# Optimization experiments

Hardware: AMD Instinct MI355X
Metric: run time of the kernel (lower is better)

## Reference

```python
import jax, jax.numpy as jnp
import numpy as np

T, B, D, U = 256, 128, 1024, 1024

def _orthogonal(key, shape, gain=1.0, dtype=jnp.float32):
    # Orthogonal init matching tf.initializers.Orthogonal
    n_rows, n_cols = shape
    big = max(n_rows, n_cols)
    a = jax.random.normal(key, (big, min(n_rows, n_cols)), dtype=jnp.float32)
    q, r = jnp.linalg.qr(a)
    q = q * jnp.sign(jnp.diag(r))
    q = q[:n_rows, :n_cols] if n_rows >= n_cols else q.T[:n_rows, :n_cols]
    return (gain * q).astype(dtype)

def setup_inputs() -> dict:
    key = jax.random.key(0)
    k1, k2, k3, k4 = jax.random.split(key, 4)
    inputs = jax.random.normal(k1, (T, B, D), dtype=jnp.float32)
    states = jnp.zeros((2, B, U), dtype=jnp.float32)  # stacked (c, h)
    masks = jax.random.randint(k2, (T, B), 0, 2).astype(jnp.int32)
    kernelx = _orthogonal(k3, (D, 4 * U), gain=1.0)
    kernelh = _orthogonal(k4, (U, 4 * U), gain=1.0)
    bias = jnp.zeros((4 * U,), dtype=jnp.float32)
    return {"inputs": inputs, "states": states, "masks": masks,
            "kernelx": kernelx, "kernelh": kernelh, "bias": bias}

def reference(inputs, states, masks, kernelx, kernelh, bias):
    c0, h0 = states[0], states[1]
    # mask semantics from source: m = 1 - masks; state is zeroed where mask==1
    m = (1.0 - masks.astype(inputs.dtype))[..., None]       # [T, B, 1]
    # Precompute input contribution for all steps (one big GEMM)
    xz = jnp.einsum('tbd,dk->tbk', inputs, kernelx) + bias  # [T, B, 4U]

    def step(carry, xs):
        c, h = carry
        xz_t, m_t = xs
        c = c * m_t
        h = h * m_t
        z = xz_t + h @ kernelh                              # [B, 4U]
        i, f, o, u = jnp.split(z, 4, axis=-1)
        i = jax.nn.sigmoid(i)
        f = jax.nn.sigmoid(f)
        o = jax.nn.sigmoid(o)
        u = jnp.tanh(u)
        c = f * c + i * u
        h = o * jnp.tanh(c)
        return (c, h), h

    (c, h), out = jax.lax.scan(step, (c0, h0), (xz, m))
    return out, jnp.stack([c, h])
```

## Files before the change

### kernel.cpp

```cpp
#include <hip/hip_runtime.h>


typedef float  f32x4 __attribute__((ext_vector_type(4)));
typedef float  f32x2 __attribute__((ext_vector_type(2)));
typedef __bf16 bf16x8 __attribute__((ext_vector_type(8)));
typedef unsigned short us8 __attribute__((ext_vector_type(8)));
typedef unsigned short us4 __attribute__((ext_vector_type(4)));
typedef unsigned int   u32x4 __attribute__((ext_vector_type(4)));

#define TT 256
#define BB 128
#define DD 1024
#define UU 1024
#define NZ 4096

typedef __attribute__((address_space(3))) unsigned       lds_u32;
typedef const __attribute__((address_space(1))) unsigned glob_u32;

__device__ __forceinline__ unsigned short f2bf(float x) {
  union { float f; unsigned u; } v; v.f = x;
  unsigned r = v.u + 0x7fffu + ((v.u >> 16) & 1u);
  return (unsigned short)(r >> 16);
}
__device__ __forceinline__ float bf2f(unsigned short b) {
  union { unsigned u; float f; } v; v.u = ((unsigned)b) << 16;
  return v.f;
}
__device__ __forceinline__ float sigm(float x) { return 1.f / (1.f + __expf(-x)); }
__device__ __forceinline__ float tanh_(float x) { return 1.f - 2.f / (__expf(2.f * x) + 1.f); }

__global__ __launch_bounds__(256) void k_convert(const float* __restrict__ in,
                                                 unsigned short* __restrict__ out,
                                                 int n8) {
  int i = blockIdx.x * 256 + threadIdx.x;
  if (i >= n8) return;
  const float4 a = *(const float4*)(in + (size_t)i * 8);
  const float4 b = *(const float4*)(in + (size_t)i * 8 + 4);
  us8 v;
  v[0] = f2bf(a.x); v[1] = f2bf(a.y); v[2] = f2bf(a.z); v[3] = f2bf(a.w);
  v[4] = f2bf(b.x); v[5] = f2bf(b.y); v[6] = f2bf(b.z); v[7] = f2bf(b.w);
  *(us8*)(out + (size_t)i * 8) = v;
}

__global__ __launch_bounds__(256) void k_transpose(const float* __restrict__ in,
                                                   unsigned short* __restrict__ out) {
  __shared__ unsigned short tile[64][72];
  const int ni = blockIdx.x;
  const int ki = blockIdx.y;
  const int t = threadIdx.x;
  const int c = t & 63, r0 = t >> 6;
#pragma unroll
  for (int rr = 0; rr < 16; ++rr) {
    int r = r0 * 16 + rr;
    tile[r][c] = f2bf(in[(size_t)(ki * 64 + r) * NZ + ni * 64 + c]);
  }
  __syncthreads();
  const int kcol = t & 63, ng = t >> 6;
#pragma unroll
  for (int cc = 0; cc < 16; ++cc) {
    int n_off = ng * 16 + cc;
    out[(size_t)(ni * 64 + n_off) * DD + ki * 64 + kcol] = tile[kcol][n_off];
  }
}

__global__ __launch_bounds__(256, 2) void k_gemm_bf(const unsigned short* __restrict__ A,
                                                    const unsigned short* __restrict__ Bt,
                                                    unsigned short* __restrict__ C) {
  __shared__ unsigned short Al[2][128 * 64];
  __shared__ unsigned short Bl[2][128 * 64];
  const int bx = blockIdx.x;
  const int wgid = (bx & 7) * 1024 + (bx >> 3);
  const int tm = wgid >> 5, tn = wgid & 31;
  const int tid = threadIdx.x;
  const int wave = tid >> 6, lane = tid & 63;
  const int wr = wave >> 1, wc = wave & 1;
  const int l15 = lane & 15, kg = lane >> 4;

  f32x4 acc[4][4] = {};

  const int srow = tid >> 3;
  const int scol = (tid & 7) * 8;
  const unsigned sdst = tid * 8;

  auto stage = [&](int buf, int kt) {
#pragma unroll
    for (int i = 0; i < 4; ++i) {
      __builtin_amdgcn_global_load_lds(
          (glob_u32*)(A  + (size_t)(tm * 128 + i * 32 + srow) * DD + kt * 64 + scol),
          (lds_u32*)&Al[buf][i * 2048 + sdst], 16, 0, 0);
      __builtin_amdgcn_global_load_lds(
          (glob_u32*)(Bt + (size_t)(tn * 128 + i * 32 + srow) * DD + kt * 64 + scol),
          (lds_u32*)&Bl[buf][i * 2048 + sdst], 16, 0, 0);
    }
  };

  stage(0, 0);
  __syncthreads();

  for (int kt = 0; kt < 16; ++kt) {
    const int buf = kt & 1;
    if (kt < 15) stage(buf ^ 1, kt + 1);
#pragma unroll
    for (int ks = 0; ks < 2; ++ks) {
      bf16x8 af[4], bfr[4];
#pragma unroll
      for (int mi = 0; mi < 4; ++mi)
        af[mi] = *(const bf16x8*)&Al[buf][(wr * 64 + mi * 16 + l15) * 64 + ks * 32 + kg * 8];
#pragma unroll
      for (int ni = 0; ni < 4; ++ni)
        bfr[ni] = *(const bf16x8*)&Bl[buf][(wc * 64 + ni * 16 + l15) * 64 + ks * 32 + kg * 8];
#pragma unroll
      for (int mi = 0; mi < 4; ++mi)
#pragma unroll
        for (int ni = 0; ni < 4; ++ni)
          acc[ni][mi] = __builtin_amdgcn_mfma_f32_16x16x32_bf16(bfr[ni], af[mi], acc[ni][mi], 0, 0, 0);
    }
    __syncthreads();
  }

#pragma unroll
  for (int mi = 0; mi < 4; ++mi) {
    const size_t row = (size_t)tm * 128 + wr * 64 + mi * 16 + l15;
#pragma unroll
    for (int ni = 0; ni < 4; ++ni) {
      const size_t col = (size_t)tn * 128 + wc * 64 + ni * 16 + kg * 4;
      us4 v;
      v[0] = f2bf(acc[ni][mi][0]); v[1] = f2bf(acc[ni][mi][1]);
      v[2] = f2bf(acc[ni][mi][2]); v[3] = f2bf(acc[ni][mi][3]);
      *(us4*)(C + row * NZ + col) = v;
    }
  }
}

__global__ __launch_bounds__(256, 1) void k_scan(const float* __restrict__ init_cs,
                                                 const int* __restrict__ masks,
                                                 const unsigned short* __restrict__ WhT,
                                                 const float* __restrict__ bias,
                                                 const unsigned short* __restrict__ xz,
                                                 float* __restrict__ out,
                                                 unsigned short* __restrict__ hglob,
                                                 unsigned* __restrict__ flags) {
  __shared__ char  hlds_c[32768];
  __shared__ float zlds[4][16][33];
  __shared__ int   mlds[TT * 16 + 16];

  const int tid = threadIdx.x;
  const int wave = tid >> 6, lane = tid & 63;
  const int l15 = lane & 15, kg = lane >> 4;
  const int blk = blockIdx.x;
  const int g = blk & 7;
  const int sb = blk >> 3;
  const int u0 = sb * 32;
  const int row0 = g * 16;
  unsigned* fl = flags + g * 64;

  u32x4 w0[32], w1[32];
  {
    const size_t r0 = (size_t)(wave * UU + u0 + l15) * DD;
    const size_t r1 = (size_t)(wave * UU + u0 + 16 + l15) * DD;
#pragma unroll
    for (int ks = 0; ks < 32; ++ks) {
      w0[ks] = *(const u32x4*)(WhT + r0 + ks * 32 + kg * 8);
      w1[ks] = *(const u32x4*)(WhT + r1 + ks * 32 + kg * 8);
    }
#pragma unroll
    for (int ks = 0; ks < 32; ++ks) {
      asm volatile("" : "+v"(w0[ks]));
      asm volatile("" : "+v"(w1[ks]));
    }
  }

  for (int i = 0; i < 16; ++i) {
    int idx = i * 256 + tid;
    mlds[idx] = masks[(size_t)(idx >> 4) * BB + row0 + (idx & 15)];
  }
  if (tid < 16) mlds[TT * 16 + tid] = 0;

  const int er = tid >> 4;
  const int ec = (tid & 15) * 2;
  const int grow = row0 + er;
  const int guu = u0 + ec;

  float bs0[4], bs1[4];
#pragma unroll
  for (int gt = 0; gt < 4; ++gt) {
    bs0[gt] = bias[gt * UU + guu];
    bs1[gt] = bias[gt * UU + guu + 1];
  }

  float cv0 = init_cs[(size_t)grow * UU + guu];
  float cv1 = init_cs[(size_t)grow * UU + guu + 1];
  float hv0 = init_cs[(size_t)BB * UU + grow * UU + guu];
  float hv1 = init_cs[(size_t)BB * UU + grow * UU + guu + 1];

  const unsigned wswz = ((unsigned)(er & 7)) << 4;
  const unsigned hoff = (unsigned)er * 2048u + ((((unsigned)guu) * 2u) ^ wswz);

  {
    int m0 = masks[grow];
    float s = m0 ? 0.f : 1.f;
    char* base = (char*)hglob + (size_t)g * 32768 + hoff;
    unsigned pv = ((unsigned)f2bf(hv1 * s) << 16) | f2bf(hv0 * s);
    *(unsigned*)base = pv;
  }
  __syncthreads();
  if (tid == 0) fl[sb] = 1;
  if (wave == 0) {
    unsigned v;
    do { v = __hip_atomic_load(&fl[lane & 31], __ATOMIC_RELAXED, __HIP_MEMORY_SCOPE_AGENT); }
    while (!__all(v >= 1));
  }
  __syncthreads();

  const unsigned rswz = ((unsigned)(l15 & 7)) << 4;
  const char* hp0 = hlds_c + l15 * 2048 + (((unsigned)(kg * 16 + 0)) ^ rswz);
  const char* hp1 = hlds_c + l15 * 2048 + (((unsigned)(kg * 16 + 64)) ^ rswz);

  for (int t = 0; t < TT; ++t) {
    {
      const char* gsrc = (const char*)hglob + ((size_t)((t & 1) * 8 + g)) * 32768;
      u32x4 sv[8];
#pragma unroll
      for (int i = 0; i < 8; ++i) {
        const char* ap = gsrc + (i * 256 + tid) * 16;
        asm volatile("global_load_dwordx4 %0, %1, off sc0" : "=v"(sv[i]) : "v"(ap));
      }
      asm volatile("s_waitcnt vmcnt(0)" ::: "memory");
      __builtin_amdgcn_sched_barrier(0);
#pragma unroll
      for (int i = 0; i < 8; ++i)
        *(u32x4*)(hlds_c + (i * 256 + tid) * 16) = sv[i];
    }
    __syncthreads();

    unsigned xzv[4];
    {
      const size_t xrow = ((size_t)(t * BB + grow)) * NZ;
#pragma unroll
      for (int gt = 0; gt < 4; ++gt)
        xzv[gt] = *(const unsigned*)(xz + xrow + gt * UU + guu);
    }

    f32x4 acc0 = {0.f, 0.f, 0.f, 0.f};
    f32x4 acc1 = {0.f, 0.f, 0.f, 0.f};
#pragma unroll
    for (int ks = 0; ks < 32; ++ks) {
      const char* p = ((ks & 1) ? hp1 : hp0) + (ks >> 1) * 128;
      bf16x8 a = *(const bf16x8*)p;
      acc0 = __builtin_amdgcn_mfma_f32_16x16x32_bf16(a, __builtin_bit_cast(bf16x8, w0[ks]), acc0, 0, 0, 0);
      acc1 = __builtin_amdgcn_mfma_f32_16x16x32_bf16(a, __builtin_bit_cast(bf16x8, w1[ks]), acc1, 0, 0, 0);
    }

#pragma unroll
    for (int j = 0; j < 4; ++j) {
      zlds[wave][kg * 4 + j][l15] = acc0[j];
      zlds[wave][kg * 4 + j][16 + l15] = acc1[j];
    }
    __syncthreads();

    const int mcur = mlds[t * 16 + er];
    const int mnxt = mlds[(t + 1) * 16 + er];
    float z0[4], z1[4];
#pragma unroll
    for (int gt = 0; gt < 4; ++gt) {
      z0[gt] = zlds[gt][er][ec]     + bs0[gt] + bf2f((unsigned short)(xzv[gt] & 0xffffu));
      z1[gt] = zlds[gt][er][ec + 1] + bs1[gt] + bf2f((unsigned short)(xzv[gt] >> 16));
    }
    const float sm = mcur ? 0.f : 1.f;
    cv0 *= sm; cv1 *= sm;
    {
      float ig = sigm(z0[0]), fg = sigm(z0[1]), og = sigm(z0[2]), ug = tanh_(z0[3]);
      cv0 = fg * cv0 + ig * ug;
      hv0 = og * tanh_(cv0);
    }
    {
      float ig = sigm(z1[0]), fg = sigm(z1[1]), og = sigm(z1[2]), ug = tanh_(z1[3]);
      cv1 = fg * cv1 + ig * ug;
      hv1 = og * tanh_(cv1);
    }

    *(f32x2*)(out + (size_t)t * (BB * UU) + (size_t)grow * UU + guu) = (f32x2){hv0, hv1};
    {
      const float sn = mnxt ? 0.f : 1.f;
      char* hdst = (char*)hglob + ((size_t)(((t + 1) & 1) * 8 + g)) * 32768 + hoff;
      unsigned pv = ((unsigned)f2bf(hv1 * sn) << 16) | f2bf(hv0 * sn);
      *(unsigned*)hdst = pv;
    }
    __syncthreads();
    if (tid == 0) fl[sb] = (unsigned)(t + 2);
    if (wave == 0) {
      const unsigned tgt = (unsigned)(t + 2);
      unsigned v;
      do { v = __hip_atomic_load(&fl[lane & 31], __ATOMIC_RELAXED, __HIP_MEMORY_SCOPE_AGENT); }
      while (!__all(v >= tgt));
    }
    __syncthreads();
  }

  float* so = out + (size_t)TT * BB * UU;
  *(f32x2*)(so + (size_t)grow * UU + guu) = (f32x2){cv0, cv1};
  *(f32x2*)(so + (size_t)BB * UU + grow * UU + guu) = (f32x2){hv0, hv1};
}

extern "C" void kernel_launch(void* const* d_in, const int* in_sizes, int n_in,
                              void* d_out, int out_size, void* d_ws, size_t ws_size,
                              hipStream_t stream) {
  const float* inputs  = (const float*)d_in[0];
  const float* states  = (const float*)d_in[1];
  const int*   masks   = (const int*)d_in[2];
  const float* kernelx = (const float*)d_in[3];
  const float* kernelh = (const float*)d_in[4];
  const float* bias    = (const float*)d_in[5];
  float* out = (float*)d_out;
  char* ws = (char*)d_ws;

  unsigned* flags       = (unsigned*)ws;
  unsigned short* hglob = (unsigned short*)(ws + 65536);
  unsigned short* WhT   = (unsigned short*)(ws + (size_t)2  * 1048576);
  unsigned short* WxT   = (unsigned short*)(ws + (size_t)10 * 1048576);
  unsigned short* Abf   = (unsigned short*)(ws + (size_t)18 * 1048576);
  unsigned short* xzbig = (unsigned short*)(ws + (size_t)82 * 1048576);

  k_transpose<<<dim3(64, 16), dim3(256), 0, stream>>>(kernelx, WxT);
  k_transpose<<<dim3(64, 16), dim3(256), 0, stream>>>(kernelh, WhT);
  k_convert<<<dim3(16384), dim3(256), 0, stream>>>(inputs, Abf, (TT * BB * DD) / 8);
  k_gemm_bf<<<dim3(8192), dim3(256), 0, stream>>>(Abf, WxT, xzbig);
  hipMemsetAsync(flags, 0, 2048, stream);
  k_scan<<<dim3(256), dim3(256), 0, stream>>>(states, masks, WhT, bias, xzbig,
                                              out, hglob, flags);
}
```

Measured before the change: 1.236 ms.

## Pipeline h-state staging into LDS by quarters, overlapping loads with MFMA

```diff
diff --git a/kernel.cpp b/kernel.cpp
--- a/kernel.cpp
+++ b/kernel.cpp
@@ -132,6 +132,24 @@
   }
 }
 
+#define SCAN_QUARTER(Q, VMSTR)                                                  \
+  {                                                                             \
+    asm volatile("s_waitcnt " VMSTR ::: "memory");                              \
+    __builtin_amdgcn_sched_barrier(0);                                          \
+    *(u32x4*)(hlds_c + sbase + (Q) * 512)         = sv[(Q) * 2];                \
+    *(u32x4*)(hlds_c + sbase + 16384 + (Q) * 512) = sv[(Q) * 2 + 1];            \
+    asm volatile("s_waitcnt lgkmcnt(0)" ::: "memory");                          \
+    __builtin_amdgcn_sched_barrier(0);                                          \
+    __builtin_amdgcn_s_barrier();                                               \
+    _Pragma("unroll")                                                           \
+    for (int ks = (Q) * 8; ks < (Q) * 8 + 8; ++ks) {                            \
+      const char* p = ((ks & 1) ? hp1 : hp0) + (ks >> 1) * 128;                 \
+      bf16x8 a = *(const bf16x8*)p;                                             \
+      acc0 = __builtin_amdgcn_mfma_f32_16x16x32_bf16(a, __builtin_bit_cast(bf16x8, w0[ks]), acc0, 0, 0, 0); \
+      acc1 = __builtin_amdgcn_mfma_f32_16x16x32_bf16(a, __builtin_bit_cast(bf16x8, w1[ks]), acc1, 0, 0, 0); \
+    }                                                                           \
+  }
+
 __global__ __launch_bounds__(256, 1) void k_scan(const float* __restrict__ init_cs,
                                                  const int* __restrict__ masks,
                                                  const unsigned short* __restrict__ WhT,
@@ -216,22 +234,26 @@
   const char* hp0 = hlds_c + l15 * 2048 + (((unsigned)(kg * 16 + 0)) ^ rswz);
   const char* hp1 = hlds_c + l15 * 2048 + (((unsigned)(kg * 16 + 64)) ^ rswz);
 
+  const unsigned sbase = ((unsigned)(tid >> 5)) * 2048u + ((unsigned)(tid & 31)) * 16u;
+
   for (int t = 0; t < TT; ++t) {
-    {
-      const char* gsrc = (const char*)hglob + ((size_t)((t & 1) * 8 + g)) * 32768;
-      u32x4 sv[8];
-#pragma unroll
-      for (int i = 0; i < 8; ++i) {
-        const char* ap = gsrc + (i * 256 + tid) * 16;
-        asm volatile("global_load_dwordx4 %0, %1, off sc0" : "=v"(sv[i]) : "v"(ap));
+    const char* gsrc = (const char*)hglob + ((size_t)((t & 1) * 8 + g)) * 32768;
+
+    u32x4 sv[8];
+#pragma unroll
+    for (int q = 0; q < 4; ++q) {
+#pragma unroll
+      for (int j = 0; j < 2; ++j) {
+        const char* ap = gsrc + sbase + j * 16384 + q * 512;
+        asm volatile("global_load_dwordx4 %0, %1, off sc0" : "=v"(sv[q * 2 + j]) : "v"(ap));
       }
-      asm volatile("s_waitcnt vmcnt(0)" ::: "memory");
-      __builtin_amdgcn_sched_barrier(0);
-#pragma unroll
-      for (int i = 0; i < 8; ++i)
-        *(u32x4*)(hlds_c + (i * 256 + tid) * 16) = sv[i];
-    }
-    __syncthreads();
+    }
+
+    f32x4 acc0 = {0.f, 0.f, 0.f, 0.f};
+    f32x4 acc1 = {0.f, 0.f, 0.f, 0.f};
+
+    SCAN_QUARTER(0, "vmcnt(6)")
+    SCAN_QUARTER(1, "vmcnt(4)")
 
     unsigned xzv[4];
     {
@@ -241,15 +263,8 @@
         xzv[gt] = *(const unsigned*)(xz + xrow + gt * UU + guu);
     }
 
-    f32x4 acc0 = {0.f, 0.f, 0.f, 0.f};
-    f32x4 acc1 = {0.f, 0.f, 0.f, 0.f};
-#pragma unroll
-    for (int ks = 0; ks < 32; ++ks) {
-      const char* p = ((ks & 1) ? hp1 : hp0) + (ks >> 1) * 128;
-      bf16x8 a = *(const bf16x8*)p;
-      acc0 = __builtin_amdgcn_mfma_f32_16x16x32_bf16(a, __builtin_bit_cast(bf16x8, w0[ks]), acc0, 0, 0, 0);
-      acc1 = __builtin_amdgcn_mfma_f32_16x16x32_bf16(a, __builtin_bit_cast(bf16x8, w1[ks]), acc1, 0, 0, 0);
-    }
+    SCAN_QUARTER(2, "vmcnt(6)")
+    SCAN_QUARTER(3, "vmcnt(4)")
 
 #pragma unroll
     for (int j = 0; j < 4; ++j) {
@@ -279,14 +294,18 @@
       hv1 = og * tanh_(cv1);
     }
 
-    *(f32x2*)(out + (size_t)t * (BB * UU) + (size_t)grow * UU + guu) = (f32x2){hv0, hv1};
     {
       const float sn = mnxt ? 0.f : 1.f;
       char* hdst = (char*)hglob + ((size_t)(((t + 1) & 1) * 8 + g)) * 32768 + hoff;
       unsigned pv = ((unsigned)f2bf(hv1 * sn) << 16) | f2bf(hv0 * sn);
-      *(unsigned*)hdst = pv;
-    }
-    __syncthreads();
+      asm volatile("global_store_dword %0, %1, off" :: "v"(hdst), "v"(pv) : "memory");
+      float* odst = out + (size_t)t * (BB * UU) + (size_t)grow * UU + guu;
+      f32x2 ov = {hv0, hv1};
+      asm volatile("global_store_dwordx2 %0, %1, off" :: "v"(odst), "v"(ov) : "memory");
+    }
+    asm volatile("s_waitcnt vmcnt(1)" ::: "memory");
+    __builtin_amdgcn_sched_barrier(0);
+    __builtin_amdgcn_s_barrier();
     if (tid == 0) fl[sb] = (unsigned)(t + 2);
     if (wave == 0) {
       const unsigned tgt = (unsigned)(t + 2);
@@ -294,7 +313,7 @@
       do { v = __hip_atomic_load(&fl[lane & 31], __ATOMIC_RELAXED, __HIP_MEMORY_SCOPE_AGENT); }
       while (!__all(v >= tgt));
     }
-    __syncthreads();
+    __builtin_amdgcn_s_barrier();
   }
 
   float* so = out + (size_t)TT * BB * UU;
```

Measured after the change: 1.199 ms, median of 2. 3.0% less time.

## Double-buffer h in LDS and restructure per-step sync in persistent LSTM scan

Applied to the files above, without the earlier changes.

```diff
diff --git a/kernel.cpp b/kernel.cpp
--- a/kernel.cpp
+++ b/kernel.cpp
@@ -140,7 +140,7 @@
                                                  float* __restrict__ out,
                                                  unsigned short* __restrict__ hglob,
                                                  unsigned* __restrict__ flags) {
-  __shared__ char  hlds_c[32768];
+  __shared__ char  hlds_c[2 * 32768];
   __shared__ float zlds[4][16][33];
   __shared__ int   mlds[TT * 16 + 16];
 
@@ -204,42 +204,48 @@
     *(unsigned*)base = pv;
   }
   __syncthreads();
-  if (tid == 0) fl[sb] = 1;
-  if (wave == 0) {
+  if (tid == 0)
+    __hip_atomic_store(&fl[sb], 1u, __ATOMIC_RELAXED, __HIP_MEMORY_SCOPE_AGENT);
+  {
     unsigned v;
     do { v = __hip_atomic_load(&fl[lane & 31], __ATOMIC_RELAXED, __HIP_MEMORY_SCOPE_AGENT); }
     while (!__all(v >= 1));
   }
-  __syncthreads();
 
   const unsigned rswz = ((unsigned)(l15 & 7)) << 4;
-  const char* hp0 = hlds_c + l15 * 2048 + (((unsigned)(kg * 16 + 0)) ^ rswz);
-  const char* hp1 = hlds_c + l15 * 2048 + (((unsigned)(kg * 16 + 64)) ^ rswz);
+
+  unsigned xz_cur[4], xz_nxt[4];
+
+  {
+    const char* gsrc = (const char*)hglob + (size_t)g * 32768;
+    u32x4 sv[8];
+#pragma unroll
+    for (int i = 0; i < 8; ++i) {
+      const char* ap = gsrc + (i * 256 + tid) * 16;
+      asm volatile("global_load_dwordx4 %0, %1, off sc0" : "=v"(sv[i]) : "v"(ap));
+    }
+    {
+      const char* xb = (const char*)xz + (((size_t)grow) * NZ + guu) * 2;
+#pragma unroll
+      for (int gt = 0; gt < 4; ++gt) {
+        const void* ap = xb + gt * (UU * 2);
+        asm volatile("global_load_dword %0, %1, off" : "=v"(xz_cur[gt]) : "v"(ap));
+      }
+    }
+    asm volatile("s_waitcnt vmcnt(4)" ::: "memory");
+    __builtin_amdgcn_sched_barrier(0);
+#pragma unroll
+    for (int i = 0; i < 8; ++i)
+      *(u32x4*)(hlds_c + (i * 256 + tid) * 16) = sv[i];
+    asm volatile("s_waitcnt lgkmcnt(0)" ::: "memory");
+    __builtin_amdgcn_sched_barrier(0);
+    __builtin_amdgcn_s_barrier();
+  }
 
   for (int t = 0; t < TT; ++t) {
-    {
-      const char* gsrc = (const char*)hglob + ((size_t)((t & 1) * 8 + g)) * 32768;
-      u32x4 sv[8];
-#pragma unroll
-      for (int i = 0; i < 8; ++i) {
-        const char* ap = gsrc + (i * 256 + tid) * 16;
-        asm volatile("global_load_dwordx4 %0, %1, off sc0" : "=v"(sv[i]) : "v"(ap));
-      }
-      asm volatile("s_waitcnt vmcnt(0)" ::: "memory");
-      __builtin_amdgcn_sched_barrier(0);
-#pragma unroll
-      for (int i = 0; i < 8; ++i)
-        *(u32x4*)(hlds_c + (i * 256 + tid) * 16) = sv[i];
-    }
-    __syncthreads();
-
-    unsigned xzv[4];
-    {
-      const size_t xrow = ((size_t)(t * BB + grow)) * NZ;
-#pragma unroll
-      for (int gt = 0; gt < 4; ++gt)
-        xzv[gt] = *(const unsigned*)(xz + xrow + gt * UU + guu);
-    }
+    const char* hb  = hlds_c + (size_t)(t & 1) * 32768;
+    const char* hp0 = hb + l15 * 2048 + (((unsigned)(kg * 16 + 0)) ^ rswz);
+    const char* hp1 = hb + l15 * 2048 + (((unsigned)(kg * 16 + 64)) ^ rswz);
 
     f32x4 acc0 = {0.f, 0.f, 0.f, 0.f};
     f32x4 acc1 = {0.f, 0.f, 0.f, 0.f};
@@ -256,15 +262,20 @@
       zlds[wave][kg * 4 + j][l15] = acc0[j];
       zlds[wave][kg * 4 + j][16 + l15] = acc1[j];
     }
-    __syncthreads();
+    asm volatile("s_waitcnt lgkmcnt(0)" ::: "memory");
+    __builtin_amdgcn_sched_barrier(0);
+    __builtin_amdgcn_s_barrier();
+
+    asm volatile("s_waitcnt vmcnt(0)" ::: "memory");
+    __builtin_amdgcn_sched_barrier(0);
 
     const int mcur = mlds[t * 16 + er];
     const int mnxt = mlds[(t + 1) * 16 + er];
     float z0[4], z1[4];
 #pragma unroll
     for (int gt = 0; gt < 4; ++gt) {
-      z0[gt] = zlds[gt][er][ec]     + bs0[gt] + bf2f((unsigned short)(xzv[gt] & 0xffffu));
-      z1[gt] = zlds[gt][er][ec + 1] + bs1[gt] + bf2f((unsigned short)(xzv[gt] >> 16));
+      z0[gt] = zlds[gt][er][ec]     + bs0[gt] + bf2f((unsigned short)(xz_cur[gt] & 0xffffu));
+      z1[gt] = zlds[gt][er][ec + 1] + bs1[gt] + bf2f((unsigned short)(xz_cur[gt] >> 16));
     }
     const float sm = mcur ? 0.f : 1.f;
     cv0 *= sm; cv1 *= sm;
@@ -279,22 +290,56 @@
       hv1 = og * tanh_(cv1);
     }
 
-    *(f32x2*)(out + (size_t)t * (BB * UU) + (size_t)grow * UU + guu) = (f32x2){hv0, hv1};
     {
       const float sn = mnxt ? 0.f : 1.f;
       char* hdst = (char*)hglob + ((size_t)(((t + 1) & 1) * 8 + g)) * 32768 + hoff;
       unsigned pv = ((unsigned)f2bf(hv1 * sn) << 16) | f2bf(hv0 * sn);
-      *(unsigned*)hdst = pv;
-    }
-    __syncthreads();
-    if (tid == 0) fl[sb] = (unsigned)(t + 2);
-    if (wave == 0) {
-      const unsigned tgt = (unsigned)(t + 2);
-      unsigned v;
-      do { v = __hip_atomic_load(&fl[lane & 31], __ATOMIC_RELAXED, __HIP_MEMORY_SCOPE_AGENT); }
-      while (!__all(v >= tgt));
-    }
-    __syncthreads();
+      asm volatile("global_store_dword %0, %1, off" :: "v"(hdst), "v"(pv) : "memory");
+      float* odst = out + (size_t)t * (BB * UU) + (size_t)grow * UU + guu;
+      f32x2 ov = {hv0, hv1};
+      asm volatile("global_store_dwordx2 %0, %1, off" :: "v"(odst), "v"(ov) : "memory");
+    }
+    asm volatile("s_waitcnt vmcnt(1)" ::: "memory");
+    __builtin_amdgcn_sched_barrier(0);
+    __builtin_amdgcn_s_barrier();
+    if (tid == 0)
+      __hip_atomic_store(&fl[sb], (unsigned)(t + 2), __ATOMIC_RELAXED, __HIP_MEMORY_SCOPE_AGENT);
+
+    if (t + 1 < TT) {
+      {
+        const unsigned tgt = (unsigned)(t + 2);
+        unsigned v;
+        do { v = __hip_atomic_load(&fl[lane & 31], __ATOMIC_RELAXED, __HIP_MEMORY_SCOPE_AGENT); }
+        while (!__all(v >= tgt));
+      }
+      const char* gsrc = (const char*)hglob + ((size_t)(((t + 1) & 1) * 8 + g)) * 32768;
+      u32x4 sv[8];
+#pragma unroll
+      for (int i = 0; i < 8; ++i) {
+        const char* ap = gsrc + (i * 256 + tid) * 16;
+        asm volatile("global_load_dwordx4 %0, %1, off sc0" : "=v"(sv[i]) : "v"(ap));
+      }
+      {
+        const char* xb = (const char*)xz + (((size_t)((t + 1) * BB + grow)) * NZ + guu) * 2;
+#pragma unroll
+        for (int gt = 0; gt < 4; ++gt) {
+          const void* ap = xb + gt * (UU * 2);
+          asm volatile("global_load_dword %0, %1, off" : "=v"(xz_nxt[gt]) : "v"(ap));
+        }
+      }
+      asm volatile("s_waitcnt vmcnt(4)" ::: "memory");
+      __builtin_amdgcn_sched_barrier(0);
+      char* ldst = hlds_c + (size_t)((t + 1) & 1) * 32768;
+#pragma unroll
+      for (int i = 0; i < 8; ++i)
+        *(u32x4*)(ldst + (i * 256 + tid) * 16) = sv[i];
+      asm volatile("s_waitcnt lgkmcnt(0)" ::: "memory");
+      __builtin_amdgcn_sched_barrier(0);
+      __builtin_amdgcn_s_barrier();
+
+#pragma unroll
+      for (int gt = 0; gt < 4; ++gt) xz_cur[gt] = xz_nxt[gt];
+    }
   }
 
   float* so = out + (size_t)TT * BB * UU;
```

New measurement: 1.545 ms. 25.0% more time.
